# Kernel tuning notes

Hardware: AMD Instinct MI355X
Metric: run time of the kernel (lower is better)

## Reference

```python
import jax, jax.numpy as jnp
import numpy as np

K = 3       # kernel_size
STRIDE = 1


def setup_inputs() -> dict:
    key = jax.random.key(0)
    k1, k2, k3 = jax.random.split(key, 3)
    B, C, H, W = 128, 64, 32, 32
    O = 64
    OH = (H - K) // STRIDE + 1  # 30
    OW = (W - K) // STRIDE + 1  # 30
    x = jax.random.normal(k1, (B, C, H, W), dtype=jnp.float32)
    weight = jax.random.normal(k2, (O, C, OH, OW, K, K), dtype=jnp.float32)
    bias = jax.random.normal(k3, (O, OH, OW), dtype=jnp.float32)
    return {"x": x, "weight": weight, "bias": bias}


def reference(x, weight, bias):
    # x: [B, C, H, W]; weight: [O, C, OH, OW, K, K]; bias: [O, OH, OW]
    O, C, OH, OW, _, _ = weight.shape
    # Extract all k x k patches in one pass: [B, C*K*K, OH, OW],
    # feature axis ordered (C, kh, kw) with spatial fastest.
    patches = jax.lax.conv_general_dilated_patches(
        x, filter_shape=(K, K), window_strides=(STRIDE, STRIDE), padding="VALID"
    )
    # Faithful to torch einsum 'bcih,coih->bo': the region's channel axis is
    # contracted against the weight's FIRST axis (nominal out_channels), and the
    # output channel is the weight's SECOND axis (requires C == O).
    # Rearrange weight -> [C*K*K (contract), O (output), OH, OW].
    w = jnp.transpose(weight, (0, 4, 5, 1, 2, 3)).reshape(C * K * K, O, OH, OW)
    out = jnp.einsum("bpij,poij->boij", patches, w) + bias[None]
    return out  # [B, O, OH, OW]
```

## Files before the change

kernel.cpp:

```cpp
#include <hip/hip_runtime.h>


#define BDIM 256

typedef __bf16 bf16x8 __attribute__((ext_vector_type(8)));
typedef float f32x4 __attribute__((ext_vector_type(4)));
typedef unsigned long long u64;

__device__ __forceinline__ unsigned short f2bf(float f) {
  union { float f; unsigned u; } v; v.f = f;
  unsigned r = v.u + 0x7fffu + ((v.u >> 16) & 1u);
  return (unsigned short)(r >> 16);
}

__device__ __forceinline__ bf16x8 mk_af(u64 lo, u64 hi) {
  union { u64 q[2]; bf16x8 v; } u;
  u.q[0] = lo; u.q[1] = hi;
  return u.v;
}


__global__ __launch_bounds__(256, 3) void lcl_kernel(
    const float* __restrict__ x, const float* __restrict__ wgt,
    const float* __restrict__ bias, float* __restrict__ out) {
  int bid = blockIdx.x;
  int xcd = bid & 7, sg = bid >> 3;
  int wg = (xcd < 4 ? xcd * 113 : 452 + (xcd - 4) * 112) + sg;
  int t    = wg >> 1;
  int half = wg & 1;
  int i   = t / 15;
  int j0  = (t % 15) * 2;
  int ij0 = i * 30 + j0;

  __shared__ __align__(16) unsigned short Bt[2 * 2 * 64 * 104];

  const int tid  = threadIdx.x;
  const int wave = tid >> 6;
  const int lane = tid & 63;
  const int lrow = lane & 15;
  const int q    = lane >> 4;

  {
    u64* zp = (u64*)Bt;
#pragma unroll
    for (int k = 0; k < 26; ++k) zp[tid + k * 256] = 0ull;
  }

  const int b_x = half * 64 + wave * 16 + lrow;
  const float* xp[3][2];
#pragma unroll
  for (int s = 0; s < 3; ++s)
#pragma unroll
    for (int tt = 0; tt < 2; ++tt) {
      int g  = s * 8 + q * 2 + tt;
      int cc = g / 3, kh = g % 3;
      xp[s][tt] = x + b_x * 65536 + cc * 1024 + (i + kh) * 32 + j0;
    }

  int p9 = lane / 9;
  int e9 = lane - p9 * 9;
  int U  = wave * 7 + p9;
  const char* wbase = (const char*)wgt + (size_t)U * 32400 +
                      (size_t)(ij0 * 9 + e9 * 2) * 4;
  int f0 = 2 * e9, f1 = f0 + 1;
  int r0 = f0 % 9, r1 = f1 % 9;
  int sl0 = (f0 / 9) * 6656 + (r0 / 3) * 4 + (r0 % 3);
  int sl1 = (f1 / 9) * 6656 + (r1 / 3) * 4 + (r1 % 3);

  float2 av[3][2][2];
  float2 wv[19];

#define LOAD_X(C0)                                                        \
  _Pragma("unroll") for (int s = 0; s < 3; ++s)                           \
  _Pragma("unroll") for (int tt = 0; tt < 2; ++tt) {                      \
    const float2* xq = (const float2*)(xp[s][tt] + (C0) * 1024);          \
    av[s][tt][0] = xq[0];                                                 \
    av[s][tt][1] = xq[1];                                                 \
  }

#define LOAD_W(C0)                                                        \
  {                                                                       \
    const char* wb = wbase + (size_t)(C0) * 2073600;                      \
    _Pragma("unroll") for (int ps = 0; ps < 18; ++ps)                     \
      wv[ps] = *(const float2*)(wb + ps * 907200);                        \
    if (U < 8) wv[18] = *(const float2*)(wb + 18 * 907200);               \
    else       wv[18] = float2{0.f, 0.f};                                 \
  }

  f32x4 acc[2][4];
#pragma unroll
  for (int a = 0; a < 2; ++a)
#pragma unroll
    for (int n = 0; n < 4; ++n) acc[a][n] = f32x4{0.f, 0.f, 0.f, 0.f};

  LOAD_X(0)
  LOAD_W(0)

  for (int chunk = 0; chunk < 8; ++chunk) {
    unsigned short* B = Bt + (chunk & 1) * 13312;

#pragma unroll
    for (int ps = 0; ps < 19; ++ps) {
      if (ps < 18 || U < 8) {
        int P  = ps * 28 + U;
        int cc = P >> 6, o = P & 63;
        int sb = cc * 12 + o * 104;
        B[sb + sl0] = f2bf(wv[ps].x);
        B[sb + sl1] = f2bf(wv[ps].y);
      }
    }

    u64 rb[3][2];
#pragma unroll
    for (int s = 0; s < 3; ++s)
#pragma unroll
      for (int tt = 0; tt < 2; ++tt) {
        unsigned short h0 = f2bf(av[s][tt][0].x);
        unsigned short h1 = f2bf(av[s][tt][0].y);
        unsigned short h2 = f2bf(av[s][tt][1].x);
        unsigned short h3 = f2bf(av[s][tt][1].y);
        rb[s][tt] = (u64)h0 | ((u64)h1 << 16) | ((u64)h2 << 32) |
                    ((u64)h3 << 48);
      }

    __syncthreads();

    if (chunk < 7) {
      LOAD_X((chunk + 1) * 8)
      LOAD_W((chunk + 1) * 8)
    }

#pragma unroll
    for (int s = 0; s < 3; ++s) {
      bf16x8 bfr[2][4];
#pragma unroll
      for (int jj = 0; jj < 2; ++jj)
#pragma unroll
        for (int nt = 0; nt < 4; ++nt)
          bfr[jj][nt] = *reinterpret_cast<const bf16x8*>(
              &B[jj * 6656 + (nt * 16 + lrow) * 104 + s * 32 + q * 8]);
#pragma unroll
      for (int jj = 0; jj < 2; ++jj) {
        u64 lo = (rb[s][0] >> (jj * 16)) & 0x0000FFFFFFFFFFFFull;
        u64 hi = (rb[s][1] >> (jj * 16)) & 0x0000FFFFFFFFFFFFull;
        bf16x8 af = mk_af(lo, hi);
#pragma unroll
        for (int nt = 0; nt < 4; ++nt)
          acc[jj][nt] = __builtin_amdgcn_mfma_f32_16x16x32_bf16(
              af, bfr[jj][nt], acc[jj][nt], 0, 0, 0);
      }
    }
  }

  const int b_out = half * 64 + wave * 16 + q * 4;
#pragma unroll
  for (int nt = 0; nt < 4; ++nt) {
    int o = nt * 16 + lrow;
    float2 bv = *(const float2*)(bias + o * 900 + ij0);
#pragma unroll
    for (int r = 0; r < 4; ++r) {
      int b = b_out + r;
      float2 res;
      res.x = acc[0][nt][r] + bv.x;
      res.y = acc[1][nt][r] + bv.y;
      *(float2*)(out + b * 57600 + o * 900 + ij0) = res;
    }
  }
}

extern "C" void kernel_launch(void* const* d_in, const int* in_sizes, int n_in,
                              void* d_out, int out_size, void* d_ws,
                              size_t ws_size, hipStream_t stream) {
  const float* x    = (const float*)d_in[0];
  const float* wgt  = (const float*)d_in[1];
  const float* bias = (const float*)d_in[2];
  float* out        = (float*)d_out;
  lcl_kernel<<<dim3(900), dim3(256), 0, stream>>>(x, wgt, bias, out);
}
```

Before: 338.8 us.

## Widen tiles to six output columns with 512-thread blocks covering all batches

Each block now handles six adjacent output columns and all 128 batch rows using 8 waves, launching 150 blocks instead of 900. Weight loads become contiguous 16-byte vector loads per lane, and x rows are loaded once and shifted to build overlapping im2col fragments for six columns. Output and bias use wider stores. The cost is a much larger LDS footprint, more accumulators per thread, and far fewer blocks, which may underfill the GPU's CUs.

```diff
diff --git a/kernel.cpp b/kernel.cpp
--- a/kernel.cpp
+++ b/kernel.cpp
@@ -1,18 +1,26 @@
 #include <hip/hip_runtime.h>
 
-
-#define BDIM 256
 
 typedef __bf16 bf16x8 __attribute__((ext_vector_type(8)));
 typedef float f32x4 __attribute__((ext_vector_type(4)));
 typedef unsigned long long u64;
+typedef unsigned int u32t;
+typedef unsigned short u16t;
 
-__device__ __forceinline__ unsigned short f2bf(float f) {
-  union { float f; unsigned u; } v; v.f = f;
-  unsigned r = v.u + 0x7fffu + ((v.u >> 16) & 1u);
-  return (unsigned short)(r >> 16);
+struct __attribute__((packed, aligned(8))) uf4 { f32x4 v; };
+struct __attribute__((packed, aligned(8))) uf2 { float2 v; };
+
+__device__ __forceinline__ u16t f2bf(float f) {
+  union { float f; u32t u; } v; v.f = f;
+  u32t r = v.u + 0x7fffu + ((v.u >> 16) & 1u);
+  return (u16t)(r >> 16);
 }
-
+__device__ __forceinline__ u32t pk2(float a, float b) {
+  return (u32t)f2bf(a) | ((u32t)f2bf(b) << 16);
+}
+__device__ __forceinline__ u64 pk3(float a, float b, float c) {
+  return (u64)f2bf(a) | ((u64)f2bf(b) << 16) | ((u64)f2bf(c) << 32);
+}
 __device__ __forceinline__ bf16x8 mk_af(u64 lo, u64 hi) {
   union { u64 q[2]; bf16x8 v; } u;
   u.q[0] = lo; u.q[1] = hi;
@@ -20,19 +28,17 @@
 }
 
 
-__global__ __launch_bounds__(256, 3) void lcl_kernel(
+__global__ __launch_bounds__(512, 2) void lcl_kernel(
     const float* __restrict__ x, const float* __restrict__ wgt,
     const float* __restrict__ bias, float* __restrict__ out) {
   int bid = blockIdx.x;
   int xcd = bid & 7, sg = bid >> 3;
-  int wg = (xcd < 4 ? xcd * 113 : 452 + (xcd - 4) * 112) + sg;
-  int t    = wg >> 1;
-  int half = wg & 1;
-  int i   = t / 15;
-  int j0  = (t % 15) * 2;
+  int t = (xcd < 6 ? xcd * 19 : 114 + (xcd - 6) * 18) + sg;
+  int i = t / 5;
+  int j0 = (t % 5) * 6;
   int ij0 = i * 30 + j0;
 
-  __shared__ __align__(16) unsigned short Bt[2 * 2 * 64 * 104];
+  __shared__ __align__(16) u16t Bt[2 * 6 * 64 * 104];
 
   const int tid  = threadIdx.x;
   const int wave = tid >> 6;
@@ -40,130 +46,128 @@
   const int lrow = lane & 15;
   const int q    = lane >> 4;
 
-  {
-    u64* zp = (u64*)Bt;
-#pragma unroll
-    for (int k = 0; k < 26; ++k) zp[tid + k * 256] = 0ull;
-  }
-
-  const int b_x = half * 64 + wave * 16 + lrow;
-  const float* xp[3][2];
+  const float* xb = x + (wave * 16 + lrow) * 65536 + i * 32 + j0;
+  int xoff[3][2];
 #pragma unroll
   for (int s = 0; s < 3; ++s)
 #pragma unroll
     for (int tt = 0; tt < 2; ++tt) {
-      int g  = s * 8 + q * 2 + tt;
-      int cc = g / 3, kh = g % 3;
-      xp[s][tt] = x + b_x * 65536 + cc * 1024 + (i + kh) * 32 + j0;
+      int g = s * 8 + q * 2 + tt, cc = g / 3, kh = g - cc * 3;
+      xoff[s][tt] = cc * 1024 + kh * 32;
     }
 
-  int p9 = lane / 9;
-  int e9 = lane - p9 * 9;
-  int U  = wave * 7 + p9;
-  const char* wbase = (const char*)wgt + (size_t)U * 32400 +
-                      (size_t)(ij0 * 9 + e9 * 2) * 4;
-  int f0 = 2 * e9, f1 = f0 + 1;
-  int r0 = f0 % 9, r1 = f1 % 9;
-  int sl0 = (f0 / 9) * 6656 + (r0 / 3) * 4 + (r0 % 3);
-  int sl1 = (f1 / 9) * 6656 + (r1 / 3) * 4 + (r1 % 3);
+  const float* wb = wgt + (size_t)wave * 518400 + lane * 8100 + ij0 * 9;
 
-  float2 av[3][2][2];
-  float2 wv[19];
+  f32x4 av[3][2][2];
+  f32x4 wv[13];
+  float2 wv2;
 
-#define LOAD_X(C0)                                                        \
-  _Pragma("unroll") for (int s = 0; s < 3; ++s)                           \
-  _Pragma("unroll") for (int tt = 0; tt < 2; ++tt) {                      \
-    const float2* xq = (const float2*)(xp[s][tt] + (C0) * 1024);          \
-    av[s][tt][0] = xq[0];                                                 \
-    av[s][tt][1] = xq[1];                                                 \
+#define GF(K) ((K) < 52 ? wv[(K) >> 2][(K)&3] : ((K) == 52 ? wv2.x : wv2.y))
+
+#define LOAD_CHUNK(C0)                                                      \
+  {                                                                         \
+    const float* xc = xb + (C0) * 1024;                                     \
+    _Pragma("unroll") for (int s = 0; s < 3; ++s)                           \
+    _Pragma("unroll") for (int tt = 0; tt < 2; ++tt) {                      \
+      const float* xq = xc + xoff[s][tt];                                   \
+      av[s][tt][0] = ((const uf4*)xq)->v;                                   \
+      av[s][tt][1] = ((const uf4*)(xq + 4))->v;                             \
+    }                                                                       \
+    const float* wq = wb + (size_t)(C0) * 518400;                           \
+    _Pragma("unroll") for (int e = 0; e < 13; ++e)                          \
+      wv[e] = ((const uf4*)(wq + e * 4))->v;                                \
+    wv2 = ((const uf2*)(wq + 52))->v;                                       \
   }
 
-#define LOAD_W(C0)                                                        \
-  {                                                                       \
-    const char* wb = wbase + (size_t)(C0) * 2073600;                      \
-    _Pragma("unroll") for (int ps = 0; ps < 18; ++ps)                     \
-      wv[ps] = *(const float2*)(wb + ps * 907200);                        \
-    if (U < 8) wv[18] = *(const float2*)(wb + 18 * 907200);               \
-    else       wv[18] = float2{0.f, 0.f};                                 \
-  }
-
-  f32x4 acc[2][4];
+  f32x4 acc[6][4];
 #pragma unroll
-  for (int a = 0; a < 2; ++a)
+  for (int a = 0; a < 6; ++a)
 #pragma unroll
     for (int n = 0; n < 4; ++n) acc[a][n] = f32x4{0.f, 0.f, 0.f, 0.f};
 
-  LOAD_X(0)
-  LOAD_W(0)
+  LOAD_CHUNK(0)
 
   for (int chunk = 0; chunk < 8; ++chunk) {
-    unsigned short* B = Bt + (chunk & 1) * 13312;
+    u16t* B = Bt + (chunk & 1) * 39936;
 
 #pragma unroll
-    for (int ps = 0; ps < 19; ++ps) {
-      if (ps < 18 || U < 8) {
-        int P  = ps * 28 + U;
-        int cc = P >> 6, o = P & 63;
-        int sb = cc * 12 + o * 104;
-        B[sb + sl0] = f2bf(wv[ps].x);
-        B[sb + sl1] = f2bf(wv[ps].y);
+    for (int dj = 0; dj < 6; ++dj) {
+      u16t* Bp = B + dj * 6656 + lane * 104 + wave * 12;
+#pragma unroll
+      for (int kh = 0; kh < 3; ++kh) {
+        const int k0 = dj * 9 + kh * 3;
+        float f0 = GF(k0), f1 = GF(k0 + 1), f2v = GF(k0 + 2);
+        *(u64*)&Bp[kh * 4] = pk3(f0, f1, f2v);
       }
     }
 
-    u64 rb[3][2];
+    u64 rb[3][2][2];
 #pragma unroll
     for (int s = 0; s < 3; ++s)
 #pragma unroll
       for (int tt = 0; tt < 2; ++tt) {
-        unsigned short h0 = f2bf(av[s][tt][0].x);
-        unsigned short h1 = f2bf(av[s][tt][0].y);
-        unsigned short h2 = f2bf(av[s][tt][1].x);
-        unsigned short h3 = f2bf(av[s][tt][1].y);
-        rb[s][tt] = (u64)h0 | ((u64)h1 << 16) | ((u64)h2 << 32) |
-                    ((u64)h3 << 48);
+        f32x4 a0 = av[s][tt][0], a1 = av[s][tt][1];
+        rb[s][tt][0] = (u64)pk2(a0[0], a0[1]) | ((u64)pk2(a0[2], a0[3]) << 32);
+        rb[s][tt][1] = (u64)pk2(a1[0], a1[1]) | ((u64)pk2(a1[2], a1[3]) << 32);
       }
 
     __syncthreads();
 
-    if (chunk < 7) {
-      LOAD_X((chunk + 1) * 8)
-      LOAD_W((chunk + 1) * 8)
-    }
+    if (chunk < 7) LOAD_CHUNK((chunk + 1) * 8)
 
 #pragma unroll
     for (int s = 0; s < 3; ++s) {
-      bf16x8 bfr[2][4];
 #pragma unroll
-      for (int jj = 0; jj < 2; ++jj)
+      for (int jj = 0; jj < 6; ++jj) {
+        bf16x8 bfr[4];
 #pragma unroll
         for (int nt = 0; nt < 4; ++nt)
-          bfr[jj][nt] = *reinterpret_cast<const bf16x8*>(
+          bfr[nt] = *reinterpret_cast<const bf16x8*>(
               &B[jj * 6656 + (nt * 16 + lrow) * 104 + s * 32 + q * 8]);
-#pragma unroll
-      for (int jj = 0; jj < 2; ++jj) {
-        u64 lo = (rb[s][0] >> (jj * 16)) & 0x0000FFFFFFFFFFFFull;
-        u64 hi = (rb[s][1] >> (jj * 16)) & 0x0000FFFFFFFFFFFFull;
+        u64 lo, hi;
+        if (jj == 0) {
+          lo = rb[s][0][0];
+          hi = rb[s][1][0];
+        } else if (jj < 4) {
+          lo = (rb[s][0][0] >> (16 * jj)) | (rb[s][0][1] << (16 * (4 - jj)));
+          hi = (rb[s][1][0] >> (16 * jj)) | (rb[s][1][1] << (16 * (4 - jj)));
+        } else if (jj == 4) {
+          lo = rb[s][0][1];
+          hi = rb[s][1][1];
+        } else {
+          lo = rb[s][0][1] >> 16;
+          hi = rb[s][1][1] >> 16;
+        }
         bf16x8 af = mk_af(lo, hi);
 #pragma unroll
         for (int nt = 0; nt < 4; ++nt)
           acc[jj][nt] = __builtin_amdgcn_mfma_f32_16x16x32_bf16(
-              af, bfr[jj][nt], acc[jj][nt], 0, 0, 0);
+              af, bfr[nt], acc[jj][nt], 0, 0, 0);
       }
     }
   }
 
-  const int b_out = half * 64 + wave * 16 + q * 4;
+  const int b_out = wave * 16 + q * 4;
 #pragma unroll
   for (int nt = 0; nt < 4; ++nt) {
     int o = nt * 16 + lrow;
-    float2 bv = *(const float2*)(bias + o * 900 + ij0);
+    const float* bp = bias + o * 900 + ij0;
+    f32x4 b03 = ((const uf4*)bp)->v;
+    float2 b45 = ((const uf2*)(bp + 4))->v;
 #pragma unroll
     for (int r = 0; r < 4; ++r) {
       int b = b_out + r;
-      float2 res;
-      res.x = acc[0][nt][r] + bv.x;
-      res.y = acc[1][nt][r] + bv.y;
-      *(float2*)(out + b * 57600 + o * 900 + ij0) = res;
+      float* op = out + b * 57600 + o * 900 + ij0;
+      f32x4 r03;
+      r03[0] = acc[0][nt][r] + b03[0];
+      r03[1] = acc[1][nt][r] + b03[1];
+      r03[2] = acc[2][nt][r] + b03[2];
+      r03[3] = acc[3][nt][r] + b03[3];
+      float2 r45;
+      r45.x = acc[4][nt][r] + b45.x;
+      r45.y = acc[5][nt][r] + b45.y;
+      ((uf4*)op)->v = r03;
+      ((uf2*)(op + 4))->v = r45;
     }
   }
 }
@@ -175,5 +179,5 @@
   const float* wgt  = (const float*)d_in[1];
   const float* bias = (const float*)d_in[2];
   float* out        = (float*)d_out;
-  lcl_kernel<<<dim3(900), dim3(256), 0, stream>>>(x, wgt, bias, out);
+  lcl_kernel<<<dim3(150), dim3(512), 0, stream>>>(x, wgt, bias, out);
 }
```

Result: no change. 338.9 us (+0.0%).
